# Performance work log

Hardware: AMD Instinct MI355X
Metric: run time of the kernel (lower is better)

## Reference

```python
import jax, jax.numpy as jnp
import numpy as np

N_ATOMS = 10000
N_HIDDEN = 75


def setup_inputs() -> dict:
    key = jax.random.key(0)
    k1, k2, k3, k4 = jax.random.split(key, 4)
    n_edges, n_pair_features = 64000, 14
    pair_features = jax.random.normal(k1, (n_edges, n_pair_features), dtype=jnp.float32)
    atom_features = jax.random.normal(k2, (N_ATOMS, N_HIDDEN), dtype=jnp.float32)
    atom_to_pair = jnp.sort(
        jax.random.randint(k3, (n_edges, 2), 0, N_ATOMS), axis=0
    ).astype(jnp.int64)
    # glorot_uniform for W [n_pair_features, n_hidden*n_hidden]
    fan_in, fan_out = n_pair_features, N_HIDDEN * N_HIDDEN
    limit = np.sqrt(6.0 / (fan_in + fan_out)).astype(np.float32)
    W = jax.random.uniform(k4, (fan_in, fan_out), minval=-limit, maxval=limit, dtype=jnp.float32)
    b = jnp.zeros((fan_out,), dtype=jnp.float32)
    return {"pair_features": pair_features, "atom_features": atom_features,
            "atom_to_pair": atom_to_pair, "W": W, "b": b}


def reference(pair_features, atom_features, atom_to_pair, W, b):
    # A: per-edge [n_hidden, n_hidden] matrices from pair features
    A = (pair_features @ W + b).reshape(-1, N_HIDDEN, N_HIDDEN)  # [E, H, H]
    # gather destination-atom features, batched matvec
    l = atom_features[atom_to_pair[:, 1]]                         # [E, H]
    out = jnp.einsum('ehk,ek->eh', A, l)                          # [E, H]
    # scatter-reduce to source atoms
    return jax.ops.segment_sum(out, atom_to_pair[:, 0], num_segments=N_ATOMS)
```

## Files before the change

kernel.cpp:

```cpp
#include <hip/hip_runtime.h>
#include <hip/hip_bf16.h>
#include <stdint.h>

constexpr int NA   = 10000;
constexpr int NH   = 75;
constexpr int NPF  = 14;
constexpr int NW   = 5625;
constexpr int NCOL = 1200;
constexpr int KP   = 104;
constexpr int MROW = 10112;
constexpr int WROW = 1208;
constexpr int JSL  = 38;
constexpr int BN   = 240;
constexpr int ACH  = 26;
constexpr int BCH  = 49;

typedef _Float16 f16;
typedef __attribute__((ext_vector_type(2))) _Float16 f16x2;
typedef __attribute__((ext_vector_type(8))) _Float16 f16x8;
typedef __attribute__((ext_vector_type(4))) float floatx4;

__device__ __forceinline__ ushort f2h_bits(float f) {
    return __builtin_bit_cast(ushort, (f16)f);
}
__device__ __forceinline__ f16x2 bch(uint32_t w) {
    return __builtin_bit_cast(f16x2, w);
}

__device__ __forceinline__ void gload16(const void* g, void* l) {
    __builtin_amdgcn_global_load_lds(
        (const __attribute__((address_space(1))) uint32_t*)g,
        (__attribute__((address_space(3))) uint32_t*)l, 16, 0, 0);
}

__device__ __forceinline__ int xcd_swz(int orig, int nwg) {
    int q = nwg >> 3, r = nwg & 7;
    int xcd = orig & 7, i = orig >> 3;
    return (xcd < r ? xcd * (q + 1) : r * (q + 1) + (xcd - r) * q) + i;
}

__device__ __forceinline__ float dot16(uint4 p0, uint4 p1, uint4 u0, uint4 u1, float c) {
    c = __builtin_amdgcn_fdot2(bch(p0.x), bch(u0.x), c, false);
    c = __builtin_amdgcn_fdot2(bch(p0.y), bch(u0.y), c, false);
    c = __builtin_amdgcn_fdot2(bch(p0.z), bch(u0.z), c, false);
    c = __builtin_amdgcn_fdot2(bch(p0.w), bch(u0.w), c, false);
    c = __builtin_amdgcn_fdot2(bch(p1.x), bch(u1.x), c, false);
    c = __builtin_amdgcn_fdot2(bch(p1.y), bch(u1.y), c, false);
    c = __builtin_amdgcn_fdot2(bch(p1.z), bch(u1.z), c, false);
    c = __builtin_amdgcn_fdot2(bch(p1.w), bch(u1.w), c, false);
    return c;
}

__global__ __launch_bounds__(256) void k_prep(
    const float* __restrict__ af, const float* __restrict__ W,
    const float* __restrict__ bias, const float* __restrict__ pf,
    const int* __restrict__ atp,
    ushort* __restrict__ afb, ushort* __restrict__ wbt,
    ushort* __restrict__ pfh, int* __restrict__ rs,
    int E, int bA, int bW, int bP)
{
    const int b = blockIdx.x, tid = threadIdx.x;
    if (b < bA) {
        int idx = b * 256 + tid;
        if (idx >= MROW * (KP / 4)) return;
        int a = idx / (KP / 4), q = idx - a * (KP / 4);
        int k0 = q * 4;
        ushort4 st = {0, 0, 0, 0};
        if (a < NA) {
            float v[4];
            #pragma unroll
            for (int j = 0; j < 4; ++j) {
                int k = k0 + j;
                v[j] = (k < NH) ? af[a * NH + k] : 0.f;
            }
            st.x = f2h_bits(v[0]); st.y = f2h_bits(v[1]);
            st.z = f2h_bits(v[2]); st.w = f2h_bits(v[3]);
        }
        ((ushort4*)afb)[idx] = st;
    } else if (b < bA + bW) {
        int idx = (b - bA) * 256 + tid;
        if (idx >= WROW * (KP / 4)) return;
        int c = idx / (KP / 4), q = idx - c * (KP / 4);
        int k0 = q * 4;
        ushort4 st = {0, 0, 0, 0};
        if (c < NCOL) {
            int h = c >> 4, f = c & 15;
            float v[4] = {0.f, 0.f, 0.f, 0.f};
            #pragma unroll
            for (int j = 0; j < 4; ++j) {
                int k = k0 + j;
                if (k < NH) {
                    if (f < NPF)       v[j] = W[f * NW + h * NH + k];
                    else if (f == NPF) v[j] = bias[h * NH + k];
                }
            }
            st.x = f2h_bits(v[0]); st.y = f2h_bits(v[1]);
            st.z = f2h_bits(v[2]); st.w = f2h_bits(v[3]);
        }
        ((ushort4*)wbt)[idx] = st;
    } else if (b < bA + bW + bP) {
        int e = (b - bA - bW) * 256 + tid;
        if (e >= E) return;
        const float* pfe = pf + (size_t)e * NPF;
        union { f16 h[16]; uint4 q[2]; } u;
        #pragma unroll
        for (int f = 0; f < 7; ++f) {
            float2 t = *(const float2*)&pfe[2 * f];
            u.h[2 * f]     = (f16)t.x;
            u.h[2 * f + 1] = (f16)t.y;
        }
        u.h[14] = (f16)1.0f;
        u.h[15] = (f16)0.0f;
        uint4* dst = (uint4*)(pfh + (size_t)e * 16);
        dst[0] = u.q[0]; dst[1] = u.q[1];
    } else {
        int e = (b - bA - bW - bP) * 256 + tid;
        if (e >= E) return;
        int c  = atp[2 * e];
        int cp = (e == 0) ? -1 : atp[2 * (e - 1)];
        for (int a = cp + 1; a <= c; ++a) rs[a] = e;
        if (e == E - 1)
            for (int a = c + 1; a <= NA; ++a) rs[a] = E;
    }
}

__global__ __launch_bounds__(256, 2) void k_gemm(const ushort* __restrict__ afb,
                                                 const ushort* __restrict__ wbt,
                                                 ushort* __restrict__ U) {
    __shared__ __align__(16) ushort sm[38400];
    ushort* As = sm;
    ushort* Bs = sm + 13312;

    const int nwg = (NCOL / BN) * (MROW / 128);
    const int swz = xcd_swz(blockIdx.x, nwg);
    const int by  = swz / (NCOL / BN);
    const int bx  = swz - by * (NCOL / BN);

    const int tid  = threadIdx.x;
    const int lane = tid & 63, wid = tid >> 6;
    const int a0 = by * 128;
    const int c0 = bx * BN;

    const char* aSrc = (const char*)(afb + (size_t)a0 * KP);
    const char* bSrc = (const char*)(wbt + (size_t)c0 * KP);

    for (int c = wid; c < ACH + BCH; c += 4) {
        if (c < ACH) gload16(aSrc + c * 1024 + lane * 16, (char*)As + c * 1024);
        else {
            int cb = c - ACH;
            gload16(bSrc + cb * 1024 + lane * 16, (char*)Bs + cb * 1024);
        }
    }
    __syncthreads();

    const int lr = lane & 15;
    const int lk = (lane >> 4) * 8;
    floatx4 acc[15][2] = {};

    #pragma unroll
    for (int ks = 0; ks < 3; ++ks) {
        f16x8 a[2], bv[15];
        #pragma unroll
        for (int mf = 0; mf < 2; ++mf)
            a[mf] = *(const f16x8*)&As[(wid * 32 + mf * 16 + lr) * KP + ks * 32 + lk];
        #pragma unroll
        for (int nf = 0; nf < 15; ++nf)
            bv[nf] = *(const f16x8*)&Bs[(nf * 16 + lr) * KP + ks * 32 + lk];
        #pragma unroll
        for (int nf = 0; nf < 15; ++nf)
            #pragma unroll
            for (int mf = 0; mf < 2; ++mf)
                acc[nf][mf] = __builtin_amdgcn_mfma_f32_16x16x32_f16(
                    bv[nf], a[mf], acc[nf][mf], 0, 0, 0);
    }

    #pragma unroll
    for (int mf = 0; mf < 2; ++mf) {
        int arow = a0 + wid * 32 + mf * 16 + lr;
        if (arow >= NA) continue;
        #pragma unroll
        for (int nf = 0; nf < 15; ++nf) {
            int cbase = c0 + nf * 16 + (lane >> 4) * 4;
            uint2 st;
            st.x = __builtin_bit_cast(uint32_t,
                     __builtin_amdgcn_cvt_pkrtz(acc[nf][mf][0], acc[nf][mf][1]));
            st.y = __builtin_bit_cast(uint32_t,
                     __builtin_amdgcn_cvt_pkrtz(acc[nf][mf][2], acc[nf][mf][3]));
            *(uint2*)&U[(size_t)arow * NCOL + cbase] = st;
        }
    }
}

__global__ __launch_bounds__(256) void k_edges2(
    const ushort* __restrict__ pfh, const int* __restrict__ atp,
    const int* __restrict__ rs, const ushort* __restrict__ U,
    float* __restrict__ out, int nwg)
{
    int blk = xcd_swz(blockIdx.x, nwg);
    int idx = blk * 256 + threadIdx.x;
    if (idx >= NA * JSL) return;
    int a = idx / JSL;
    int j = idx - a * JSL;
    const bool two = (j + JSL) < NH;
    int e0 = rs[a], e1 = rs[a + 1];

    float acc0 = 0.f, acc1 = 0.f;
    for (int e = e0; e < e1; ++e) {
        int a1 = atp[2 * e + 1];
        const uint4* pq = (const uint4*)(pfh + (size_t)e * 16);
        uint4 p0 = pq[0], p1 = pq[1];
        const ushort* ub = U + (size_t)a1 * NCOL;
        {
            const uint4* up = (const uint4*)(ub + j * 16);
            acc0 = dot16(p0, p1, up[0], up[1], acc0);
        }
        if (two) {
            const uint4* up = (const uint4*)(ub + (j + JSL) * 16);
            acc1 = dot16(p0, p1, up[0], up[1], acc1);
        }
    }
    out[a * NH + j] = acc0;
    if (two) out[a * NH + j + JSL] = acc1;
}

__global__ void k_naive(const float* __restrict__ pf, const float* __restrict__ af,
                        const int* __restrict__ atp, const float* __restrict__ W,
                        const float* __restrict__ bias, float* __restrict__ out, int E)
{
    int idx = blockIdx.x * blockDim.x + threadIdx.x;
    if (idx >= E * NH) return;
    int e = idx / NH, h = idx - e * NH;
    int a0 = atp[2 * e], a1 = atp[2 * e + 1];
    float p[NPF];
    #pragma unroll
    for (int f = 0; f < NPF; ++f) p[f] = pf[(size_t)e * NPF + f];
    float acc = 0.f;
    for (int k = 0; k < NH; ++k) {
        float w = bias[h * NH + k];
        #pragma unroll
        for (int f = 0; f < NPF; ++f) w += p[f] * W[f * NW + h * NH + k];
        acc += w * af[a1 * NH + k];
    }
    atomicAdd(&out[a0 * NH + h], acc);
}

extern "C" void kernel_launch(void* const* d_in, const int* in_sizes, int n_in,
                              void* d_out, int out_size, void* d_ws, size_t ws_size,
                              hipStream_t stream) {
    const float* pf   = (const float*)d_in[0];
    const float* af   = (const float*)d_in[1];
    const int*   atp  = (const int*)d_in[2];
    const float* W    = (const float*)d_in[3];
    const float* bias = (const float*)d_in[4];
    float* out = (float*)d_out;
    const int E = in_sizes[2] / 2;

    const size_t offAfb = 0;
    const size_t offWbt = offAfb + (size_t)MROW * KP * 2;
    const size_t offU   = offWbt + (size_t)WROW * KP * 2;
    const size_t offPfh = offU + (size_t)NA * NCOL * 2;
    const size_t offRs  = offPfh + (size_t)E * 16 * 2;
    const size_t need   = offRs + (size_t)(NA + 1) * sizeof(int);

    if (ws_size >= need) {
        ushort* afb = (ushort*)((char*)d_ws + offAfb);
        ushort* wbt = (ushort*)((char*)d_ws + offWbt);
        ushort* U   = (ushort*)((char*)d_ws + offU);
        ushort* pfh = (ushort*)((char*)d_ws + offPfh);
        int*    rs  = (int*)((char*)d_ws + offRs);

        const int bA = (MROW * (KP / 4) + 255) / 256;
        const int bW = (WROW * (KP / 4) + 255) / 256;
        const int bP = (E + 255) / 256;
        const int bR = (E + 255) / 256;
        k_prep<<<bA + bW + bP + bR, 256, 0, stream>>>(af, W, bias, pf, atp,
                                                      afb, wbt, pfh, rs, E, bA, bW, bP);

        k_gemm<<<(NCOL / BN) * (MROW / 128), 256, 0, stream>>>(afb, wbt, U);

        const int nwg2 = (NA * JSL + 255) / 256;
        k_edges2<<<nwg2, 256, 0, stream>>>(pfh, atp, rs, U, out, nwg2);
    } else {
        hipMemsetAsync(d_out, 0, (size_t)out_size * sizeof(float), stream);
        k_naive<<<((size_t)E * NH + 255) / 256, 256, 0, stream>>>(pf, af, atp, W, bias, out, E);
    }
}
```

Baseline: 34.79 us.

## Stage edge windows in LDS and map 16 atoms per block in edge kernel

Replaces the per-thread edge kernel with a windowed version. Each block handles 16 consecutive source atoms, with 16 threads per atom each covering up to 5 output columns. Pair features and destination indices for the block's edge range are staged cooperatively into shared memory in chunks of 128, so redundant global loads across threads disappear. This adds block-wide syncs and can leave threads idle when edge counts vary between atoms in a block.

```diff
diff --git a/kernel.cpp b/kernel.cpp
--- a/kernel.cpp
+++ b/kernel.cpp
@@ -10,10 +10,11 @@
 constexpr int KP   = 104;
 constexpr int MROW = 10112;
 constexpr int WROW = 1208;
-constexpr int JSL  = 38;
 constexpr int BN   = 240;
 constexpr int ACH  = 26;
 constexpr int BCH  = 49;
+constexpr int EWIN = 16;
+constexpr int ECH  = 128;
 
 typedef _Float16 f16;
 typedef __attribute__((ext_vector_type(2))) _Float16 f16x2;
@@ -191,36 +192,56 @@
     }
 }
 
-__global__ __launch_bounds__(256) void k_edges2(
+__global__ __launch_bounds__(256) void k_edges_win(
     const ushort* __restrict__ pfh, const int* __restrict__ atp,
     const int* __restrict__ rs, const ushort* __restrict__ U,
-    float* __restrict__ out, int nwg)
+    float* __restrict__ out)
 {
-    int blk = xcd_swz(blockIdx.x, nwg);
-    int idx = blk * 256 + threadIdx.x;
-    if (idx >= NA * JSL) return;
-    int a = idx / JSL;
-    int j = idx - a * JSL;
-    const bool two = (j + JSL) < NH;
-    int e0 = rs[a], e1 = rs[a + 1];
-
-    float acc0 = 0.f, acc1 = 0.f;
-    for (int e = e0; e < e1; ++e) {
-        int a1 = atp[2 * e + 1];
-        const uint4* pq = (const uint4*)(pfh + (size_t)e * 16);
-        uint4 p0 = pq[0], p1 = pq[1];
-        const ushort* ub = U + (size_t)a1 * NCOL;
-        {
-            const uint4* up = (const uint4*)(ub + j * 16);
-            acc0 = dot16(p0, p1, up[0], up[1], acc0);
-        }
-        if (two) {
-            const uint4* up = (const uint4*)(ub + (j + JSL) * 16);
-            acc1 = dot16(p0, p1, up[0], up[1], acc1);
-        }
-    }
-    out[a * NH + j] = acc0;
-    if (two) out[a * NH + j + JSL] = acc1;
+    __shared__ uint4 pfs[ECH][2];
+    __shared__ int   a1s[ECH];
+
+    const int tid = threadIdx.x;
+    const int blk = xcd_swz(blockIdx.x, NA / EWIN);
+    const int ab0 = blk * EWIN;
+    const int al  = tid >> 4, j = tid & 15;
+    const int a   = ab0 + al;
+
+    const int e0w = rs[ab0], e1w = rs[ab0 + EWIN];
+    const int e0  = rs[a],   e1  = rs[a + 1];
+
+    float acc[5] = {};
+    for (int cs = e0w; cs < e1w; cs += ECH) {
+        int n = e1w - cs; if (n > ECH) n = ECH;
+        __syncthreads();
+        for (int i = tid; i < n * 2; i += 256)
+            pfs[i >> 1][i & 1] = *(const uint4*)(pfh + (size_t)(cs + (i >> 1)) * 16 + (i & 1) * 8);
+        for (int i = tid; i < n; i += 256)
+            a1s[i] = atp[2 * (cs + i) + 1];
+        __syncthreads();
+
+        int lo = e0 > cs ? e0 : cs;
+        int hi = e1 < cs + n ? e1 : cs + n;
+        for (int e = lo; e < hi; ++e) {
+            int el = e - cs;
+            uint4 p0 = pfs[el][0], p1 = pfs[el][1];
+            const ushort* ub = U + (size_t)a1s[el] * NCOL + j * 16;
+            #pragma unroll
+            for (int r = 0; r < 4; ++r) {
+                const uint4* up = (const uint4*)(ub + r * 256);
+                acc[r] = dot16(p0, p1, up[0], up[1], acc[r]);
+            }
+            if (j < NH - 64) {
+                const uint4* up = (const uint4*)(ub + 4 * 256);
+                acc[4] = dot16(p0, p1, up[0], up[1], acc[4]);
+            }
+        }
+    }
+
+    #pragma unroll
+    for (int r = 0; r < 4; ++r)
+        out[(size_t)a * NH + j + 16 * r] = acc[r];
+    if (j < NH - 64)
+        out[(size_t)a * NH + j + 64] = acc[4];
 }
 
 __global__ void k_naive(const float* __restrict__ pf, const float* __restrict__ af,
@@ -278,8 +299,7 @@
 
         k_gemm<<<(NCOL / BN) * (MROW / 128), 256, 0, stream>>>(afb, wbt, U);
 
-        const int nwg2 = (NA * JSL + 255) / 256;
-        k_edges2<<<nwg2, 256, 0, stream>>>(pfh, atp, rs, U, out, nwg2);
+        k_edges_win<<<NA / EWIN, 256, 0, stream>>>(pfh, atp, rs, U, out);
     } else {
         hipMemsetAsync(d_out, 0, (size_t)out_size * sizeof(float), stream);
         k_naive<<<((size_t)E * NH + 255) / 256, 256, 0, stream>>>(pf, af, atp, W, bias, out, E);
```

Measured after the change: 36.92 us. 1.06x slower.

## Fuse fp16 conversion of atom features and W into GEMM kernel

Applied to the files above, without the earlier changes.

Removes the separate conversion pass that wrote padded fp16 copies of atom features and the transposed W/bias matrix to workspace. The GEMM blocks now read fp32 inputs directly, convert them and write them into LDS, and share one launch with the pair-feature and row-start prep work. This saves a kernel launch and a global round-trip of the converted operands. In exchange, W is reconverted by every row-block with scalar strided loads instead of async global-to-LDS copies, and the GEMM blocks' LDS footprint now applies to the prep blocks too.

```diff
diff --git a/kernel.cpp b/kernel.cpp
--- a/kernel.cpp
+++ b/kernel.cpp
@@ -9,11 +9,9 @@
 constexpr int NCOL = 1200;
 constexpr int KP   = 104;
 constexpr int MROW = 10112;
-constexpr int WROW = 1208;
+constexpr int BN   = 240;
+constexpr int NGB  = (NCOL / BN) * (MROW / 128);
 constexpr int JSL  = 38;
-constexpr int BN   = 240;
-constexpr int ACH  = 26;
-constexpr int BCH  = 49;
 
 typedef _Float16 f16;
 typedef __attribute__((ext_vector_type(2))) _Float16 f16x2;
@@ -25,12 +23,6 @@
 }
 __device__ __forceinline__ f16x2 bch(uint32_t w) {
     return __builtin_bit_cast(f16x2, w);
-}
-
-__device__ __forceinline__ void gload16(const void* g, void* l) {
-    __builtin_amdgcn_global_load_lds(
-        (const __attribute__((address_space(1))) uint32_t*)g,
-        (__attribute__((address_space(3))) uint32_t*)l, 16, 0, 0);
 }
 
 __device__ __forceinline__ int xcd_swz(int orig, int nwg) {
@@ -51,55 +43,85 @@
     return c;
 }
 
-__global__ __launch_bounds__(256) void k_prep(
+__global__ __launch_bounds__(256, 2) void k_main(
     const float* __restrict__ af, const float* __restrict__ W,
     const float* __restrict__ bias, const float* __restrict__ pf,
     const int* __restrict__ atp,
-    ushort* __restrict__ afb, ushort* __restrict__ wbt,
-    ushort* __restrict__ pfh, int* __restrict__ rs,
-    int E, int bA, int bW, int bP)
+    ushort* __restrict__ U, ushort* __restrict__ pfh, int* __restrict__ rs,
+    int E, int bP)
 {
+    __shared__ __align__(16) ushort sm[38400];
     const int b = blockIdx.x, tid = threadIdx.x;
-    if (b < bA) {
-        int idx = b * 256 + tid;
-        if (idx >= MROW * (KP / 4)) return;
-        int a = idx / (KP / 4), q = idx - a * (KP / 4);
-        int k0 = q * 4;
-        ushort4 st = {0, 0, 0, 0};
-        if (a < NA) {
-            float v[4];
-            #pragma unroll
-            for (int j = 0; j < 4; ++j) {
-                int k = k0 + j;
-                v[j] = (k < NH) ? af[a * NH + k] : 0.f;
+
+    if (b < NGB) {
+        ushort* As = sm;
+        ushort* Bs = sm + 13312;
+
+        const int swz = xcd_swz(b, NGB);
+        const int by  = swz / (NCOL / BN);
+        const int bx  = swz - by * (NCOL / BN);
+        const int lane = tid & 63, wid = tid >> 6;
+        const int a0 = by * 128;
+        const int c0 = bx * BN;
+
+        for (int i = tid; i < 128 * KP; i += 256) {
+            int row = i / KP, k = i - row * KP;
+            int ga = a0 + row;
+            float v = 0.f;
+            if (k < NH && ga < NA) v = af[ga * NH + k];
+            As[i] = f2h_bits(v);
+        }
+        for (int i = tid; i < BN * KP; i += 256) {
+            int c = i / KP, k = i - c * KP;
+            int gc = c0 + c;
+            int h = gc >> 4, f = gc & 15;
+            float v = 0.f;
+            if (k < NH) {
+                if (f < NPF)       v = W[f * NW + h * NH + k];
+                else if (f == NPF) v = bias[h * NH + k];
             }
-            st.x = f2h_bits(v[0]); st.y = f2h_bits(v[1]);
-            st.z = f2h_bits(v[2]); st.w = f2h_bits(v[3]);
-        }
-        ((ushort4*)afb)[idx] = st;
-    } else if (b < bA + bW) {
-        int idx = (b - bA) * 256 + tid;
-        if (idx >= WROW * (KP / 4)) return;
-        int c = idx / (KP / 4), q = idx - c * (KP / 4);
-        int k0 = q * 4;
-        ushort4 st = {0, 0, 0, 0};
-        if (c < NCOL) {
-            int h = c >> 4, f = c & 15;
-            float v[4] = {0.f, 0.f, 0.f, 0.f};
-            #pragma unroll
-            for (int j = 0; j < 4; ++j) {
-                int k = k0 + j;
-                if (k < NH) {
-                    if (f < NPF)       v[j] = W[f * NW + h * NH + k];
-                    else if (f == NPF) v[j] = bias[h * NH + k];
-                }
+            Bs[i] = f2h_bits(v);
+        }
+        __syncthreads();
+
+        const int lr = lane & 15;
+        const int lk = (lane >> 4) * 8;
+        floatx4 acc[15][2] = {};
+
+        #pragma unroll
+        for (int ks = 0; ks < 3; ++ks) {
+            f16x8 a[2], bv[15];
+            #pragma unroll
+            for (int mf = 0; mf < 2; ++mf)
+                a[mf] = *(const f16x8*)&As[(wid * 32 + mf * 16 + lr) * KP + ks * 32 + lk];
+            #pragma unroll
+            for (int nf = 0; nf < 15; ++nf)
+                bv[nf] = *(const f16x8*)&Bs[(nf * 16 + lr) * KP + ks * 32 + lk];
+            #pragma unroll
+            for (int nf = 0; nf < 15; ++nf)
+                #pragma unroll
+                for (int mf = 0; mf < 2; ++mf)
+                    acc[nf][mf] = __builtin_amdgcn_mfma_f32_16x16x32_f16(
+                        bv[nf], a[mf], acc[nf][mf], 0, 0, 0);
+        }
+
+        #pragma unroll
+        for (int mf = 0; mf < 2; ++mf) {
+            int arow = a0 + wid * 32 + mf * 16 + lr;
+            if (arow >= NA) continue;
+            #pragma unroll
+            for (int nf = 0; nf < 15; ++nf) {
+                int cbase = c0 + nf * 16 + (lane >> 4) * 4;
+                uint2 st;
+                st.x = __builtin_bit_cast(uint32_t,
+                         __builtin_amdgcn_cvt_pkrtz(acc[nf][mf][0], acc[nf][mf][1]));
+                st.y = __builtin_bit_cast(uint32_t,
+                         __builtin_amdgcn_cvt_pkrtz(acc[nf][mf][2], acc[nf][mf][3]));
+                *(uint2*)&U[(size_t)arow * NCOL + cbase] = st;
             }
-            st.x = f2h_bits(v[0]); st.y = f2h_bits(v[1]);
-            st.z = f2h_bits(v[2]); st.w = f2h_bits(v[3]);
-        }
-        ((ushort4*)wbt)[idx] = st;
-    } else if (b < bA + bW + bP) {
-        int e = (b - bA - bW) * 256 + tid;
+        }
+    } else if (b < NGB + bP) {
+        int e = (b - NGB) * 256 + tid;
         if (e >= E) return;
         const float* pfe = pf + (size_t)e * NPF;
         union { f16 h[16]; uint4 q[2]; } u;
@@ -114,80 +136,13 @@
         uint4* dst = (uint4*)(pfh + (size_t)e * 16);
         dst[0] = u.q[0]; dst[1] = u.q[1];
     } else {
-        int e = (b - bA - bW - bP) * 256 + tid;
+        int e = (b - NGB - bP) * 256 + tid;
         if (e >= E) return;
         int c  = atp[2 * e];
         int cp = (e == 0) ? -1 : atp[2 * (e - 1)];
         for (int a = cp + 1; a <= c; ++a) rs[a] = e;
         if (e == E - 1)
             for (int a = c + 1; a <= NA; ++a) rs[a] = E;
-    }
-}
-
-__global__ __launch_bounds__(256, 2) void k_gemm(const ushort* __restrict__ afb,
-                                                 const ushort* __restrict__ wbt,
-                                                 ushort* __restrict__ U) {
-    __shared__ __align__(16) ushort sm[38400];
-    ushort* As = sm;
-    ushort* Bs = sm + 13312;
-
-    const int nwg = (NCOL / BN) * (MROW / 128);
-    const int swz = xcd_swz(blockIdx.x, nwg);
-    const int by  = swz / (NCOL / BN);
-    const int bx  = swz - by * (NCOL / BN);
-
-    const int tid  = threadIdx.x;
-    const int lane = tid & 63, wid = tid >> 6;
-    const int a0 = by * 128;
-    const int c0 = bx * BN;
-
-    const char* aSrc = (const char*)(afb + (size_t)a0 * KP);
-    const char* bSrc = (const char*)(wbt + (size_t)c0 * KP);
-
-    for (int c = wid; c < ACH + BCH; c += 4) {
-        if (c < ACH) gload16(aSrc + c * 1024 + lane * 16, (char*)As + c * 1024);
-        else {
-            int cb = c - ACH;
-            gload16(bSrc + cb * 1024 + lane * 16, (char*)Bs + cb * 1024);
-        }
-    }
-    __syncthreads();
-
-    const int lr = lane & 15;
-    const int lk = (lane >> 4) * 8;
-    floatx4 acc[15][2] = {};
-
-    #pragma unroll
-    for (int ks = 0; ks < 3; ++ks) {
-        f16x8 a[2], bv[15];
-        #pragma unroll
-        for (int mf = 0; mf < 2; ++mf)
-            a[mf] = *(const f16x8*)&As[(wid * 32 + mf * 16 + lr) * KP + ks * 32 + lk];
-        #pragma unroll
-        for (int nf = 0; nf < 15; ++nf)
-            bv[nf] = *(const f16x8*)&Bs[(nf * 16 + lr) * KP + ks * 32 + lk];
-        #pragma unroll
-        for (int nf = 0; nf < 15; ++nf)
-            #pragma unroll
-            for (int mf = 0; mf < 2; ++mf)
-                acc[nf][mf] = __builtin_amdgcn_mfma_f32_16x16x32_f16(
-                    bv[nf], a[mf], acc[nf][mf], 0, 0, 0);
-    }
-
-    #pragma unroll
-    for (int mf = 0; mf < 2; ++mf) {
-        int arow = a0 + wid * 32 + mf * 16 + lr;
-        if (arow >= NA) continue;
-        #pragma unroll
-        for (int nf = 0; nf < 15; ++nf) {
-            int cbase = c0 + nf * 16 + (lane >> 4) * 4;
-            uint2 st;
-            st.x = __builtin_bit_cast(uint32_t,
-                     __builtin_amdgcn_cvt_pkrtz(acc[nf][mf][0], acc[nf][mf][1]));
-            st.y = __builtin_bit_cast(uint32_t,
-                     __builtin_amdgcn_cvt_pkrtz(acc[nf][mf][2], acc[nf][mf][3]));
-            *(uint2*)&U[(size_t)arow * NCOL + cbase] = st;
-        }
     }
 }
 
@@ -255,28 +210,20 @@
     float* out = (float*)d_out;
     const int E = in_sizes[2] / 2;
 
-    const size_t offAfb = 0;
-    const size_t offWbt = offAfb + (size_t)MROW * KP * 2;
-    const size_t offU   = offWbt + (size_t)WROW * KP * 2;
+    const size_t offU   = 0;
     const size_t offPfh = offU + (size_t)NA * NCOL * 2;
     const size_t offRs  = offPfh + (size_t)E * 16 * 2;
     const size_t need   = offRs + (size_t)(NA + 1) * sizeof(int);
 
     if (ws_size >= need) {
-        ushort* afb = (ushort*)((char*)d_ws + offAfb);
-        ushort* wbt = (ushort*)((char*)d_ws + offWbt);
         ushort* U   = (ushort*)((char*)d_ws + offU);
         ushort* pfh = (ushort*)((char*)d_ws + offPfh);
         int*    rs  = (int*)((char*)d_ws + offRs);
 
-        const int bA = (MROW * (KP / 4) + 255) / 256;
-        const int bW = (WROW * (KP / 4) + 255) / 256;
         const int bP = (E + 255) / 256;
         const int bR = (E + 255) / 256;
-        k_prep<<<bA + bW + bP + bR, 256, 0, stream>>>(af, W, bias, pf, atp,
-                                                      afb, wbt, pfh, rs, E, bA, bW, bP);
-
-        k_gemm<<<(NCOL / BN) * (MROW / 128), 256, 0, stream>>>(afb, wbt, U);
+        k_main<<<NGB + bP + bR, 256, 0, stream>>>(af, W, bias, pf, atp,
+                                                  U, pfh, rs, E, bP);
 
         const int nwg2 = (NA * JSL + 255) / 256;
         k_edges2<<<nwg2, 256, 0, stream>>>(pfh, atp, rs, U, out, nwg2);
```

After: 75.54 us. 2.17x slower.
